# Kernel optimization log

Measured on AMD Instinct MI355X. Metric: run time of the kernel, lower is better.

Reference implementation:

```python
import jax, jax.numpy as jnp
import numpy as np

N = 100000   # node_num
E = 1000000  # num edges
D = 256      # input_dim
H = 256      # hidden_dim


def setup_inputs() -> dict:
    key = jax.random.key(0)
    ks = jax.random.split(key, 6)
    x = jax.random.uniform(ks[0], (N, D), dtype=jnp.float32)  # nn.Parameter rand init
    edge_index = jax.random.randint(ks[1], (2, E), 0, N, dtype=jnp.int64)
    W1 = jax.random.normal(ks[2], (D, H), dtype=jnp.float32) * (1.0 / np.sqrt(D))
    b1 = jnp.zeros((H,), dtype=jnp.float32)
    W2 = jax.random.normal(ks[3], (H, H), dtype=jnp.float32) * (1.0 / np.sqrt(H))
    b2 = jnp.zeros((H,), dtype=jnp.float32)
    return {"edge_index": edge_index, "x": x, "W1": W1, "b1": b1, "W2": W2, "b2": b2}


def reference(edge_index, x, W1, b1, W2, b2):
    # GCNConv: add self-loops, symmetric normalization D^-1/2 (A+I) D^-1/2,
    # then (norm-weighted scatter-add of x@W) + bias, followed by ReLU.
    src, dst = edge_index[0], edge_index[1]
    loops = jnp.arange(N, dtype=src.dtype)
    s = jnp.concatenate([src, loops])          # [E+N] message sources
    d = jnp.concatenate([dst, loops])          # [E+N] message targets
    w = jnp.ones((E + N,), dtype=jnp.float32)  # edge_weight = 1 (incl. self-loops)
    deg = jax.ops.segment_sum(w, d, num_segments=N)
    dinv = jnp.where(deg > 0, jax.lax.rsqrt(deg), 0.0)
    norm = dinv[s] * w * dinv[d]               # [E+N]

    def layer(z, W, b):
        h = z @ W                                               # [N, H]
        agg = jax.ops.segment_sum(norm[:, None] * h[s], d, num_segments=N)
        return jax.nn.relu(agg + b)

    z = layer(x, W1, b1)
    z = layer(z, W2, b2)
    return z
```

## Files before the change

kernel.cpp:

```cpp
#include <hip/hip_runtime.h>
#include <stdint.h>

#define N_NODES 100000
#define N_EDGES 1000000
#define DIM 256
#define CAP 32

typedef __attribute__((ext_vector_type(8))) short short8;
typedef __attribute__((ext_vector_type(8))) unsigned short u16x8;
typedef __attribute__((ext_vector_type(4))) float f32x4;
typedef __attribute__((ext_vector_type(4))) unsigned short u16x4;

__device__ inline float b2f(unsigned short u) {
    union { unsigned int i; float f; } v; v.i = ((unsigned int)u) << 16; return v.f;
}
__device__ inline unsigned short f2b(float f) {
    union { float f; unsigned int i; } v; v.f = f;
    unsigned int u = v.i;
    return (unsigned short)((u + 0x7FFFu + ((u >> 16) & 1u)) >> 16);
}


#define NB_FILL 489
#define NB_PACK 512
#define NB_CVT  25000

__global__ void k_pre(const int* __restrict__ src, const int* __restrict__ dst,
                      uint32_t* __restrict__ cnt, uint32_t* __restrict__ ovfCnt,
                      int* __restrict__ colM, uint32_t* __restrict__ ovf,
                      const float* __restrict__ W1, const float* __restrict__ W2,
                      unsigned short* __restrict__ Wt1, unsigned short* __restrict__ Wt2,
                      const float* __restrict__ x, unsigned short* __restrict__ xs) {
    int b = blockIdx.x, t = threadIdx.x;
    if (b < NB_FILL) {
        int e = b * 2048 + t;
        #pragma unroll
        for (int k = 0; k < 8; ++k, e += 256) {
            if (e < N_EDGES) {
                unsigned d = (unsigned)dst[e];
                unsigned s = (unsigned)src[e];
                if (d < N_NODES && s < N_NODES) {
                    uint32_t p = atomicAdd(&cnt[d], 1u);
                    if (p < CAP) colM[(size_t)d * CAP + p] = (int)s;
                    else {
                        uint32_t o = atomicAdd(ovfCnt, 1u);
                        if (o < (uint32_t)N_EDGES) { ovf[2 * o] = d; ovf[2 * o + 1] = s; }
                    }
                }
            }
        }
    } else if (b < NB_FILL + NB_PACK) {
        int n = b - NB_FILL;
        if (n < 256) Wt1[n * 256 + t] = f2b(W1[t * 256 + n]);
        else { n -= 256; Wt2[n * 256 + t] = f2b(W2[t * 256 + n]); }
    } else {
        int i = (b - (NB_FILL + NB_PACK)) * 256 + t;
        f32x4 v = __builtin_nontemporal_load((const f32x4*)x + i);
        u16x4 o;
        o.x = f2b(v.x); o.y = f2b(v.y); o.z = f2b(v.z); o.w = f2b(v.w);
        *((u16x4*)xs + i) = o;
    }
}

__global__ void k_wgt(const uint32_t* __restrict__ cnt, float* __restrict__ wgt) {
    int n = blockIdx.x * blockDim.x + threadIdx.x;
    if (n < N_NODES) wgt[n] = rsqrtf((float)(cnt[n] + 1u));
}

__global__ __launch_bounds__(256, 4) void k_fused(
        const unsigned short* __restrict__ rows, const uint32_t* __restrict__ cnt,
        const float* __restrict__ wgt,
        const uint32_t* __restrict__ ovfCnt, const int* __restrict__ colM,
        const uint32_t* __restrict__ ovf, const unsigned short* __restrict__ Wt,
        const float* __restrict__ bias,
        unsigned short* __restrict__ Cb, float* __restrict__ Cf) {
    __shared__ __align__(16) unsigned short As[64 * 256];

    int tid = threadIdx.x;
    int w = tid >> 6, lane = tid & 63;
    int hl = lane & 31, half = lane >> 5;
    int rowBase = blockIdx.x * 64;
    uint32_t ovfN = *ovfCnt;

    const u16x8* r8 = (const u16x8*)rows;
    #pragma unroll 1
    for (int t = 0; t < 8; ++t) {
        int nl    = w * 16 + t * 2 + half;
        int node  = rowBase + nl;
        bool valid = node < N_NODES;
        int nsafe = valid ? node : 0;

        uint32_t dgRaw = cnt[nsafe];
        float    di    = wgt[nsafe];
        uint32_t dg    = valid ? (dgRaw < CAP ? dgRaw : CAP) : 0u;
        float    wSelf = valid ? di : 0.f;

        u16x8 sv = r8[(size_t)nsafe * 32 + hl];
        float a[8];
        #pragma unroll
        for (int i = 0; i < 8; ++i) a[i] = wSelf * b2f(sv[i]);

        uint32_t dgo   = (uint32_t)__shfl((int)dg, lane ^ 32);
        uint32_t dgMax = dg > dgo ? dg : dgo;
        const int* cp  = colM + (size_t)nsafe * CAP;

        for (uint32_t j = 0; j < dgMax; j += 8) {
            int4 i0 = *(const int4*)(cp + j);
            int4 i1 = *(const int4*)(cp + j + 4);
            unsigned x0 = min((unsigned)i0.x, N_NODES - 1u);
            unsigned x1 = min((unsigned)i0.y, N_NODES - 1u);
            unsigned x2 = min((unsigned)i0.z, N_NODES - 1u);
            unsigned x3 = min((unsigned)i0.w, N_NODES - 1u);
            unsigned x4 = min((unsigned)i1.x, N_NODES - 1u);
            unsigned x5 = min((unsigned)i1.y, N_NODES - 1u);
            unsigned x6 = min((unsigned)i1.z, N_NODES - 1u);
            unsigned x7 = min((unsigned)i1.w, N_NODES - 1u);
            u16x8 r0 = r8[(size_t)x0 * 32 + hl];
            u16x8 r1 = r8[(size_t)x1 * 32 + hl];
            u16x8 r2 = r8[(size_t)x2 * 32 + hl];
            u16x8 r3 = r8[(size_t)x3 * 32 + hl];
            u16x8 r4 = r8[(size_t)x4 * 32 + hl];
            u16x8 r5 = r8[(size_t)x5 * 32 + hl];
            u16x8 r6 = r8[(size_t)x6 * 32 + hl];
            u16x8 r7 = r8[(size_t)x7 * 32 + hl];
            float w0 = (j + 0 < dg) ? wgt[x0] : 0.f;
            float w1 = (j + 1 < dg) ? wgt[x1] : 0.f;
            float w2 = (j + 2 < dg) ? wgt[x2] : 0.f;
            float w3 = (j + 3 < dg) ? wgt[x3] : 0.f;
            float w4 = (j + 4 < dg) ? wgt[x4] : 0.f;
            float w5 = (j + 5 < dg) ? wgt[x5] : 0.f;
            float w6 = (j + 6 < dg) ? wgt[x6] : 0.f;
            float w7 = (j + 7 < dg) ? wgt[x7] : 0.f;
            #pragma unroll
            for (int i = 0; i < 8; ++i) {
                float s = fmaf(w0, b2f(r0[i]), a[i]);
                s = fmaf(w1, b2f(r1[i]), s);
                s = fmaf(w2, b2f(r2[i]), s);
                s = fmaf(w3, b2f(r3[i]), s);
                s = fmaf(w4, b2f(r4[i]), s);
                s = fmaf(w5, b2f(r5[i]), s);
                s = fmaf(w6, b2f(r6[i]), s);
                s = fmaf(w7, b2f(r7[i]), s);
                a[i] = s;
            }
        }

        if (ovfN) {
            for (uint32_t k = 0; k < ovfN; ++k) {
                uint32_t od = ovf[2 * k], os = ovf[2 * k + 1];
                if (valid && od == (uint32_t)node) {
                    float wv = wgt[os];
                    u16x8 rv = r8[(size_t)os * 32 + hl];
                    #pragma unroll
                    for (int i = 0; i < 8; ++i) a[i] = fmaf(wv, b2f(rv[i]), a[i]);
                }
            }
        }

        short8 o;
        #pragma unroll
        for (int i = 0; i < 8; ++i) o[i] = (short)f2b(di * a[i]);
        *(short8*)((char*)As + nl * 512 + ((hl ^ (nl & 7)) << 4)) = o;
    }
    __syncthreads();

    int m = lane & 15, quad = lane >> 4;

    f32x4 acc[4][4];
    #pragma unroll
    for (int mt = 0; mt < 4; ++mt)
        #pragma unroll
        for (int nt = 0; nt < 4; ++nt)
            acc[mt][nt] = (f32x4){0.f, 0.f, 0.f, 0.f};

    #pragma unroll
    for (int ks = 0; ks < 8; ++ks) {
        short8 wf[4], xf[4];
        #pragma unroll
        for (int nt = 0; nt < 4; ++nt)
            wf[nt] = *(const short8*)(Wt + (size_t)(w * 64 + nt * 16 + m) * 256 + ks * 32 + quad * 8);
        #pragma unroll
        for (int mt = 0; mt < 4; ++mt) {
            int rl = mt * 16 + m;
            int ch = (ks * 4 + quad) ^ (rl & 7);
            xf[mt] = *(const short8*)((const char*)As + rl * 512 + (ch << 4));
        }
        #pragma unroll
        for (int mt = 0; mt < 4; ++mt)
            #pragma unroll
            for (int nt = 0; nt < 4; ++nt)
                acc[mt][nt] = __builtin_amdgcn_mfma_f32_16x16x32_bf16(
                    wf[nt], xf[mt], acc[mt][nt], 0, 0, 0);
    }

    float4 bv[4];
    #pragma unroll
    for (int nt = 0; nt < 4; ++nt)
        bv[nt] = *(const float4*)(bias + w * 64 + nt * 16 + quad * 4);

    #pragma unroll
    for (int mt = 0; mt < 4; ++mt) {
        int node = rowBase + mt * 16 + m;
        if (node >= N_NODES) continue;
        if (Cf) {
            #pragma unroll
            for (int nt = 0; nt < 4; ++nt) {
                int c = w * 64 + nt * 16 + quad * 4;
                f32x4 v = acc[mt][nt];
                f32x4 o;
                o.x = fmaxf(v[0] + bv[nt].x, 0.f);
                o.y = fmaxf(v[1] + bv[nt].y, 0.f);
                o.z = fmaxf(v[2] + bv[nt].z, 0.f);
                o.w = fmaxf(v[3] + bv[nt].w, 0.f);
                __builtin_nontemporal_store(o, (f32x4*)(Cf + (size_t)node * 256 + c));
            }
        } else {
            #pragma unroll
            for (int nt = 0; nt < 4; ++nt) {
                int c = w * 64 + nt * 16 + quad * 4;
                f32x4 v = acc[mt][nt];
                u16x4 o;
                o.x = f2b(fmaxf(v[0] + bv[nt].x, 0.f));
                o.y = f2b(fmaxf(v[1] + bv[nt].y, 0.f));
                o.z = f2b(fmaxf(v[2] + bv[nt].z, 0.f));
                o.w = f2b(fmaxf(v[3] + bv[nt].w, 0.f));
                *(u16x4*)(Cb + (size_t)node * 256 + c) = o;
            }
        }
    }
}

extern "C" void kernel_launch(void* const* d_in, const int* in_sizes, int n_in,
                              void* d_out, int out_size, void* d_ws, size_t ws_size,
                              hipStream_t stream) {
    const int*   edge = (const int*)d_in[0];
    const float* x    = (const float*)d_in[1];
    const float* W1   = (const float*)d_in[2];
    const float* b1   = (const float*)d_in[3];
    const float* W2   = (const float*)d_in[4];
    const float* b2   = (const float*)d_in[5];
    float* out = (float*)d_out;

    char* ws = (char*)d_ws;
    uint32_t*       cnt    = (uint32_t*)(ws + 0);
    uint32_t*       ovfCnt = (uint32_t*)(ws + 400000);
    int*            colM   = (int*)     (ws + 400256);
    float*          wgt    = (float*)   (ws + 13200256);
    uint32_t*       ovf    = (uint32_t*)(ws + 13600256);
    unsigned short* Wt1    = (unsigned short*)(ws + 21600256);
    unsigned short* Wt2    = (unsigned short*)(ws + 21731328);
    unsigned short* xs     = (unsigned short*)(ws + 21862400);
    unsigned short* z1s    = (unsigned short*)(ws + 73062400ull);

    const int* src = edge;
    const int* dst = edge + N_EDGES;

    hipMemsetAsync(ws, 0, 400256, stream);

    k_pre<<<NB_FILL + NB_PACK + NB_CVT, 256, 0, stream>>>(
        src, dst, cnt, ovfCnt, colM, ovf, W1, W2, Wt1, Wt2, x, xs);
    k_wgt<<<(N_NODES + 255) / 256, 256, 0, stream>>>(cnt, wgt);

    k_fused<<<(N_NODES + 63) / 64, 256, 0, stream>>>(
        xs, cnt, wgt, ovfCnt, colM, ovf, Wt1, b1, z1s, nullptr);
    k_fused<<<(N_NODES + 63) / 64, 256, 0, stream>>>(
        z1s, cnt, wgt, ovfCnt, colM, ovf, Wt2, b2, nullptr, out);
}
```

Measured before the change: 437.9 us.

## Split fused gather+GEMM into separate gather and GEMM kernels per layer

Unfuses the aggregation from the MFMA GEMM. A new wave-per-node gather kernel runs at higher occupancy and writes a bf16 aggregate buffer, then a plain GEMM kernel reads it back. The aim is to stop the latency-bound gather from being held to the GEMM kernel's occupancy, and to remove the half-wave divergence on degree. The cost is an extra 51MB round trip to global memory per layer and two more launches. The edge-fill blocks are also resized to 4096 edges each.

```diff
diff --git a/kernel.cpp b/kernel.cpp
--- a/kernel.cpp
+++ b/kernel.cpp
@@ -7,7 +7,6 @@
 #define CAP 32
 
 typedef __attribute__((ext_vector_type(8))) short short8;
-typedef __attribute__((ext_vector_type(8))) unsigned short u16x8;
 typedef __attribute__((ext_vector_type(4))) float f32x4;
 typedef __attribute__((ext_vector_type(4))) unsigned short u16x4;
 
@@ -21,7 +20,7 @@
 }
 
 
-#define NB_FILL 489
+#define NB_FILL 245
 #define NB_PACK 512
 #define NB_CVT  25000
 
@@ -33,9 +32,9 @@
                       const float* __restrict__ x, unsigned short* __restrict__ xs) {
     int b = blockIdx.x, t = threadIdx.x;
     if (b < NB_FILL) {
-        int e = b * 2048 + t;
-        #pragma unroll
-        for (int k = 0; k < 8; ++k, e += 256) {
+        int e = b * 4096 + t;
+        #pragma unroll
+        for (int k = 0; k < 16; ++k, e += 256) {
             if (e < N_EDGES) {
                 unsigned d = (unsigned)dst[e];
                 unsigned s = (unsigned)src[e];
@@ -67,100 +66,104 @@
     if (n < N_NODES) wgt[n] = rsqrtf((float)(cnt[n] + 1u));
 }
 
-__global__ __launch_bounds__(256, 4) void k_fused(
+__global__ __launch_bounds__(256, 8) void k_gather(
         const unsigned short* __restrict__ rows, const uint32_t* __restrict__ cnt,
         const float* __restrict__ wgt,
         const uint32_t* __restrict__ ovfCnt, const int* __restrict__ colM,
-        const uint32_t* __restrict__ ovf, const unsigned short* __restrict__ Wt,
+        const uint32_t* __restrict__ ovf, unsigned short* __restrict__ out) {
+    int wave = threadIdx.x >> 6, lane = threadIdx.x & 63;
+    int node = blockIdx.x * 4 + wave;
+    const u16x4* r4 = (const u16x4*)rows;
+
+    uint32_t dgRaw = cnt[node];
+    float    di    = wgt[node];
+    uint32_t dg    = dgRaw < CAP ? dgRaw : CAP;
+    uint32_t ovfN  = *ovfCnt;
+
+    u16x4 sv = r4[(size_t)node * 64 + lane];
+    float a[4];
+    a[0] = di * b2f(sv.x); a[1] = di * b2f(sv.y);
+    a[2] = di * b2f(sv.z); a[3] = di * b2f(sv.w);
+
+    const int* cp = colM + (size_t)node * CAP;
+    for (uint32_t j = 0; j < dg; j += 8) {
+        int4 i0 = *(const int4*)(cp + j);
+        int4 i1 = *(const int4*)(cp + j + 4);
+        unsigned x0 = min((unsigned)i0.x, N_NODES - 1u);
+        unsigned x1 = min((unsigned)i0.y, N_NODES - 1u);
+        unsigned x2 = min((unsigned)i0.z, N_NODES - 1u);
+        unsigned x3 = min((unsigned)i0.w, N_NODES - 1u);
+        unsigned x4 = min((unsigned)i1.x, N_NODES - 1u);
+        unsigned x5 = min((unsigned)i1.y, N_NODES - 1u);
+        unsigned x6 = min((unsigned)i1.z, N_NODES - 1u);
+        unsigned x7 = min((unsigned)i1.w, N_NODES - 1u);
+        u16x4 r0 = r4[(size_t)x0 * 64 + lane];
+        u16x4 r1 = r4[(size_t)x1 * 64 + lane];
+        u16x4 r2 = r4[(size_t)x2 * 64 + lane];
+        u16x4 r3 = r4[(size_t)x3 * 64 + lane];
+        u16x4 r4v = r4[(size_t)x4 * 64 + lane];
+        u16x4 r5 = r4[(size_t)x5 * 64 + lane];
+        u16x4 r6 = r4[(size_t)x6 * 64 + lane];
+        u16x4 r7 = r4[(size_t)x7 * 64 + lane];
+        float w0 = (j + 0 < dg) ? wgt[x0] : 0.f;
+        float w1 = (j + 1 < dg) ? wgt[x1] : 0.f;
+        float w2 = (j + 2 < dg) ? wgt[x2] : 0.f;
+        float w3 = (j + 3 < dg) ? wgt[x3] : 0.f;
+        float w4 = (j + 4 < dg) ? wgt[x4] : 0.f;
+        float w5 = (j + 5 < dg) ? wgt[x5] : 0.f;
+        float w6 = (j + 6 < dg) ? wgt[x6] : 0.f;
+        float w7 = (j + 7 < dg) ? wgt[x7] : 0.f;
+        #pragma unroll
+        for (int i = 0; i < 4; ++i) {
+            float s = fmaf(w0, b2f(r0[i]), a[i]);
+            s = fmaf(w1, b2f(r1[i]), s);
+            s = fmaf(w2, b2f(r2[i]), s);
+            s = fmaf(w3, b2f(r3[i]), s);
+            s = fmaf(w4, b2f(r4v[i]), s);
+            s = fmaf(w5, b2f(r5[i]), s);
+            s = fmaf(w6, b2f(r6[i]), s);
+            s = fmaf(w7, b2f(r7[i]), s);
+            a[i] = s;
+        }
+    }
+
+    if (ovfN) {
+        for (uint32_t k = 0; k < ovfN; ++k) {
+            uint32_t od = ovf[2 * k], os = ovf[2 * k + 1];
+            if (od == (uint32_t)node) {
+                float wv = wgt[os];
+                u16x4 rv = r4[(size_t)os * 64 + lane];
+                #pragma unroll
+                for (int i = 0; i < 4; ++i) a[i] = fmaf(wv, b2f(rv[i]), a[i]);
+            }
+        }
+    }
+
+    u16x4 o;
+    o.x = f2b(di * a[0]); o.y = f2b(di * a[1]);
+    o.z = f2b(di * a[2]); o.w = f2b(di * a[3]);
+    ((u16x4*)out)[(size_t)node * 64 + lane] = o;
+}
+
+__global__ __launch_bounds__(256, 4) void k_gemm(
+        const unsigned short* __restrict__ A, const unsigned short* __restrict__ Wt,
         const float* __restrict__ bias,
         unsigned short* __restrict__ Cb, float* __restrict__ Cf) {
     __shared__ __align__(16) unsigned short As[64 * 256];
 
     int tid = threadIdx.x;
     int w = tid >> 6, lane = tid & 63;
-    int hl = lane & 31, half = lane >> 5;
     int rowBase = blockIdx.x * 64;
-    uint32_t ovfN = *ovfCnt;
-
-    const u16x8* r8 = (const u16x8*)rows;
-    #pragma unroll 1
-    for (int t = 0; t < 8; ++t) {
-        int nl    = w * 16 + t * 2 + half;
-        int node  = rowBase + nl;
-        bool valid = node < N_NODES;
-        int nsafe = valid ? node : 0;
-
-        uint32_t dgRaw = cnt[nsafe];
-        float    di    = wgt[nsafe];
-        uint32_t dg    = valid ? (dgRaw < CAP ? dgRaw : CAP) : 0u;
-        float    wSelf = valid ? di : 0.f;
-
-        u16x8 sv = r8[(size_t)nsafe * 32 + hl];
-        float a[8];
-        #pragma unroll
-        for (int i = 0; i < 8; ++i) a[i] = wSelf * b2f(sv[i]);
-
-        uint32_t dgo   = (uint32_t)__shfl((int)dg, lane ^ 32);
-        uint32_t dgMax = dg > dgo ? dg : dgo;
-        const int* cp  = colM + (size_t)nsafe * CAP;
-
-        for (uint32_t j = 0; j < dgMax; j += 8) {
-            int4 i0 = *(const int4*)(cp + j);
-            int4 i1 = *(const int4*)(cp + j + 4);
-            unsigned x0 = min((unsigned)i0.x, N_NODES - 1u);
-            unsigned x1 = min((unsigned)i0.y, N_NODES - 1u);
-            unsigned x2 = min((unsigned)i0.z, N_NODES - 1u);
-            unsigned x3 = min((unsigned)i0.w, N_NODES - 1u);
-            unsigned x4 = min((unsigned)i1.x, N_NODES - 1u);
-            unsigned x5 = min((unsigned)i1.y, N_NODES - 1u);
-            unsigned x6 = min((unsigned)i1.z, N_NODES - 1u);
-            unsigned x7 = min((unsigned)i1.w, N_NODES - 1u);
-            u16x8 r0 = r8[(size_t)x0 * 32 + hl];
-            u16x8 r1 = r8[(size_t)x1 * 32 + hl];
-            u16x8 r2 = r8[(size_t)x2 * 32 + hl];
-            u16x8 r3 = r8[(size_t)x3 * 32 + hl];
-            u16x8 r4 = r8[(size_t)x4 * 32 + hl];
-            u16x8 r5 = r8[(size_t)x5 * 32 + hl];
-            u16x8 r6 = r8[(size_t)x6 * 32 + hl];
-            u16x8 r7 = r8[(size_t)x7 * 32 + hl];
-            float w0 = (j + 0 < dg) ? wgt[x0] : 0.f;
-            float w1 = (j + 1 < dg) ? wgt[x1] : 0.f;
-            float w2 = (j + 2 < dg) ? wgt[x2] : 0.f;
-            float w3 = (j + 3 < dg) ? wgt[x3] : 0.f;
-            float w4 = (j + 4 < dg) ? wgt[x4] : 0.f;
-            float w5 = (j + 5 < dg) ? wgt[x5] : 0.f;
-            float w6 = (j + 6 < dg) ? wgt[x6] : 0.f;
-            float w7 = (j + 7 < dg) ? wgt[x7] : 0.f;
-            #pragma unroll
-            for (int i = 0; i < 8; ++i) {
-                float s = fmaf(w0, b2f(r0[i]), a[i]);
-                s = fmaf(w1, b2f(r1[i]), s);
-                s = fmaf(w2, b2f(r2[i]), s);
-                s = fmaf(w3, b2f(r3[i]), s);
-                s = fmaf(w4, b2f(r4[i]), s);
-                s = fmaf(w5, b2f(r5[i]), s);
-                s = fmaf(w6, b2f(r6[i]), s);
-                s = fmaf(w7, b2f(r7[i]), s);
-                a[i] = s;
-            }
-        }
-
-        if (ovfN) {
-            for (uint32_t k = 0; k < ovfN; ++k) {
-                uint32_t od = ovf[2 * k], os = ovf[2 * k + 1];
-                if (valid && od == (uint32_t)node) {
-                    float wv = wgt[os];
-                    u16x8 rv = r8[(size_t)os * 32 + hl];
-                    #pragma unroll
-                    for (int i = 0; i < 8; ++i) a[i] = fmaf(wv, b2f(rv[i]), a[i]);
-                }
-            }
-        }
-
-        short8 o;
-        #pragma unroll
-        for (int i = 0; i < 8; ++i) o[i] = (short)f2b(di * a[i]);
-        *(short8*)((char*)As + nl * 512 + ((hl ^ (nl & 7)) << 4)) = o;
+
+    #pragma unroll
+    for (int i = 0; i < 8; ++i) {
+        int c  = tid + i * 256;
+        int r  = c >> 5;
+        int kb = c & 31;
+        int gr = rowBase + r;
+        int4 v = {0, 0, 0, 0};
+        if (gr < N_NODES) v = *(const int4*)(A + (size_t)gr * 256 + kb * 8);
+        *(int4*)((char*)As + r * 512 + ((kb ^ (r & 7)) << 4)) = v;
     }
     __syncthreads();
 
@@ -251,6 +254,7 @@
     unsigned short* Wt2    = (unsigned short*)(ws + 21731328);
     unsigned short* xs     = (unsigned short*)(ws + 21862400);
     unsigned short* z1s    = (unsigned short*)(ws + 73062400ull);
+    unsigned short* agg    = (unsigned short*)(ws + 124262400ull);
 
     const int* src = edge;
     const int* dst = edge + N_EDGES;
@@ -261,8 +265,8 @@
         src, dst, cnt, ovfCnt, colM, ovf, W1, W2, Wt1, Wt2, x, xs);
     k_wgt<<<(N_NODES + 255) / 256, 256, 0, stream>>>(cnt, wgt);
 
-    k_fused<<<(N_NODES + 63) / 64, 256, 0, stream>>>(
-        xs, cnt, wgt, ovfCnt, colM, ovf, Wt1, b1, z1s, nullptr);
-    k_fused<<<(N_NODES + 63) / 64, 256, 0, stream>>>(
-        z1s, cnt, wgt, ovfCnt, colM, ovf, Wt2, b2, nullptr, out);
-}
+    k_gather<<<N_NODES / 4, 256, 0, stream>>>(xs, cnt, wgt, ovfCnt, colM, ovf, agg);
+    k_gemm<<<(N_NODES + 63) / 64, 256, 0, stream>>>(agg, Wt1, b1, z1s, nullptr);
+    k_gather<<<N_NODES / 4, 256, 0, stream>>>(z1s, cnt, wgt, ovfCnt, colM, ovf, agg);
+    k_gemm<<<(N_NODES + 63) / 64, 256, 0, stream>>>(agg, Wt2, b2, nullptr, out);
+}
```

Result: slower. 468.2 us (+6.9%).
